# Kernel tuning notes

Hardware: AMD Instinct MI355X
Metric: run time of the kernel (lower is better)

Reference implementation:

```python
import jax, jax.numpy as jnp
import numpy as np

N = 100000   # nodes
E = 1250000  # edges
IN, HID, OUT = 64, 128, 32


def _gcn_norm(edge_index, num_nodes):
    # add self loops, unit edge weights, symmetric normalization (PyG gcn_norm)
    loops = jnp.arange(num_nodes, dtype=edge_index.dtype)
    src = jnp.concatenate([edge_index[0], loops])
    dst = jnp.concatenate([edge_index[1], loops])
    w = jnp.ones(src.shape[0], dtype=jnp.float32)
    deg = jax.ops.segment_sum(w, dst, num_segments=num_nodes)  # degree at targets
    dis = jnp.where(deg > 0, jax.lax.rsqrt(deg), 0.0)
    norm = dis[src] * dis[dst]  # per-edge coefficient
    return src, dst, norm


def _gcn_conv(h, W, b, src, dst, norm, num_nodes):
    hw = h @ W                                 # [N, out] linear transform first
    msg = hw[src] * norm[:, None]              # gather + scale  [E+N, out]
    agg = jax.ops.segment_sum(msg, dst, num_segments=num_nodes)
    return agg + b


def setup_inputs() -> dict:
    key = jax.random.key(0)
    ks = jax.random.split(key, 8)
    x = jax.random.normal(ks[0], (N, IN), dtype=jnp.float32)
    edge_index = jax.random.randint(ks[1], (2, E), 0, N, dtype=jnp.int32)
    def glorot(k, fan_in, fan_out):
        s = np.sqrt(6.0 / (fan_in + fan_out)).astype(np.float32)
        return jax.random.uniform(k, (fan_in, fan_out), jnp.float32, -s, s)
    return {
        "x": x,
        "edge_index": edge_index,
        "W1": glorot(ks[2], IN, HID),   "b1": jnp.zeros((HID,), jnp.float32),
        "W_mu": glorot(ks[3], HID, OUT), "b_mu": jnp.zeros((OUT,), jnp.float32),
        "W_lv": glorot(ks[4], HID, OUT), "b_lv": jnp.zeros((OUT,), jnp.float32),
    }


def reference(x, edge_index, W1, b1, W_mu, b_mu, W_lv, b_lv):
    src, dst, norm = _gcn_norm(edge_index, N)
    h = _gcn_conv(x, W1, b1, src, dst, norm, N)
    h = jax.nn.selu(h)
    # dropout: eval mode (training=False) -> identity
    mu = _gcn_conv(h, W_mu, b_mu, src, dst, norm, N)
    logvar = _gcn_conv(h, W_lv, b_lv, src, dst, norm, N)
    return (mu, logvar)
```

## Files before the change

### kernel.cpp

```cpp
#include <hip/hip_runtime.h>
#include <math.h>

#define NN 100000
#define NE 1250000
#define DIN 64
#define DHID 128
#define DO2 64
#define DOUT 32

#define NBIN 256
#define BINW ((NN + NBIN - 1) / NBIN)
#define PADW2 2752
#define P1_THREADS 1024
#define P1_EPT 8
#define P1_EPB (P1_THREADS * P1_EPT)

typedef unsigned int uint;
typedef unsigned short ushort;
typedef __attribute__((ext_vector_type(8))) short bf16x8;
typedef __attribute__((ext_vector_type(4))) float f32x4;

#define MFMA16(A, B, C) __builtin_amdgcn_mfma_f32_16x16x32_bf16(A, B, C, 0, 0, 0)

__device__ __forceinline__ ushort f2bf(float f) {
    uint u = __float_as_uint(f);
    uint r = (u + 0x7fffu + ((u >> 16) & 1u)) >> 16;
    return (ushort)r;
}
__device__ __forceinline__ uint pack2(float a, float b) {
    return (uint)f2bf(a) | ((uint)f2bf(b) << 16);
}
__device__ __forceinline__ float bflo(uint p) { return __uint_as_float(p << 16); }
__device__ __forceinline__ float bfhi(uint p) { return __uint_as_float(p & 0xffff0000u); }

__device__ __forceinline__ int nofk(int k) {
    return (k & 3) | (((k >> 3) & 3) << 2) | (((k >> 2) & 1) << 4) | ((k >> 5) << 5);
}

__global__ void zero_arr(int* a, int n) {
    int i = blockIdx.x * blockDim.x + threadIdx.x;
    if (i < n) a[i] = 0;
}

__global__ void cast_x(const float* __restrict__ x, const float* __restrict__ dis,
                       uint* __restrict__ xb, int npairs) {
    int i = blockIdx.x * blockDim.x + threadIdx.x;
    if (i < npairs) {
        int row = i >> 5;
        if (row < NN) {
            float dv = dis[row];
            float2 v = ((const float2*)x)[i];
            xb[i] = pack2(dv * v.x, dv * v.y);
        } else xb[i] = 0;
    }
}

__global__ __launch_bounds__(P1_THREADS) void bin_hist(const int* __restrict__ dst,
                                                       int* __restrict__ binhist, int n) {
    __shared__ int hist[NBIN];
    int tid = threadIdx.x;
    if (tid < NBIN) hist[tid] = 0;
    __syncthreads();
    int base = blockIdx.x * P1_EPB;
#pragma unroll
    for (int j = 0; j < P1_EPT; j++) {
        int i = base + j * P1_THREADS + tid;
        if (i < n) atomicAdd(&hist[dst[i] / BINW], 1);
    }
    __syncthreads();
    if (tid < NBIN) {
        int v = hist[tid];
        if (v) atomicAdd(&binhist[tid], v);
    }
}

__global__ __launch_bounds__(NBIN) void bin_scan(const int* __restrict__ binhist,
                                                 int* __restrict__ binoff,
                                                 int* __restrict__ bincur) {
    __shared__ int buf[NBIN];
    int tid = threadIdx.x;
    int v = binhist[tid];
    buf[tid] = v;
    __syncthreads();
    for (int off = 1; off < NBIN; off <<= 1) {
        int t = (tid >= off) ? buf[tid - off] : 0;
        __syncthreads();
        buf[tid] += t;
        __syncthreads();
    }
    int ex = buf[tid] - v;
    binoff[tid] = ex;
    bincur[tid] = ex;
    if (tid == NBIN - 1) binoff[NBIN] = buf[tid];
}

__global__ __launch_bounds__(P1_THREADS) void scatter_pass1(const int* __restrict__ src,
                                                            const int* __restrict__ dst,
                                                            int* __restrict__ bincur,
                                                            uint* __restrict__ ebin, int n) {
    __shared__ int hist[NBIN];
    __shared__ int gbase[NBIN];
    int tid = threadIdx.x;
    if (tid < NBIN) hist[tid] = 0;
    __syncthreads();
    int base = blockIdx.x * P1_EPB;
    uint e[P1_EPT];
    int  rk[P1_EPT];
    int  bn[P1_EPT];
#pragma unroll
    for (int j = 0; j < P1_EPT; j++) {
        int i = base + j * P1_THREADS + tid;
        if (i < n) {
            int d = dst[i];
            int b = d / BINW;
            e[j] = ((uint)src[i] << 9) | (uint)(d - b * BINW);
            bn[j] = b;
            rk[j] = atomicAdd(&hist[b], 1);
        } else bn[j] = -1;
    }
    __syncthreads();
    if (tid < NBIN) gbase[tid] = hist[tid] ? atomicAdd(&bincur[tid], hist[tid]) : 0;
    __syncthreads();
#pragma unroll
    for (int j = 0; j < P1_EPT; j++)
        if (bn[j] >= 0) ebin[gbase[bn[j]] + rk[j]] = e[j];
}

__global__ __launch_bounds__(256) void bin_finalize(const uint* __restrict__ ebin,
                                                    const int* __restrict__ binoff,
                                                    float* __restrict__ dis,
                                                    int* __restrict__ poffsets,
                                                    int* __restrict__ pends,
                                                    int* __restrict__ esrc) {
    __shared__ int hh[BINW];
    __shared__ int base_s[BINW];
    __shared__ int cur_s[BINW];
    int b = blockIdx.x;
    int tid = threadIdx.x;
    int v0 = b * BINW;
    int nv = min(BINW, NN - v0);
    int beg = binoff[b], end = binoff[b + 1];
    int pbase = ((beg + 7) & ~7) + PADW2 * b;
    for (int i = tid; i < nv; i += 256) { hh[i] = 0; cur_s[i] = 0; }
    __syncthreads();
    for (int i = beg + tid; i < end; i += 256)
        atomicAdd(&hh[ebin[i] & 511u], 1);
    __syncthreads();
    int i1 = tid + 256;
    int c0 = (tid < nv) ? hh[tid] : 0;  int p0 = (c0 + 7) & ~7;
    int c1 = (i1 < nv) ? hh[i1] : 0;    int p1 = (c1 + 7) & ~7;
    __syncthreads();
    if (tid < nv) hh[tid] = p0;
    if (i1 < nv) hh[i1] = p1;
    __syncthreads();
    for (int off = 1; off < BINW; off <<= 1) {
        int t0 = (tid < nv && tid >= off) ? hh[tid - off] : 0;
        int t1 = (i1 < nv && i1 >= off) ? hh[i1 - off] : 0;
        __syncthreads();
        if (tid < nv) hh[tid] += t0;
        if (i1 < nv) hh[i1] += t1;
        __syncthreads();
    }
    if (tid < nv) {
        int base = pbase + hh[tid] - p0;
        base_s[tid] = base;
        poffsets[v0 + tid] = base;
        pends[v0 + tid] = base + p0;
        dis[v0 + tid] = rsqrtf((float)c0 + 1.0f);
        for (int j = c0; j < p0; j++) esrc[base + j] = NN;
    }
    if (i1 < nv) {
        int base = pbase + hh[i1] - p1;
        base_s[i1] = base;
        poffsets[v0 + i1] = base;
        pends[v0 + i1] = base + p1;
        dis[v0 + i1] = rsqrtf((float)c1 + 1.0f);
        for (int j = c1; j < p1; j++) esrc[base + j] = NN;
    }
    __syncthreads();
    for (int i = beg + tid; i < end; i += 256) {
        uint e = ebin[i];
        int l = (int)(e & 511u);
        int pos = base_s[l] + atomicAdd(&cur_s[l], 1);
        esrc[pos] = (int)(e >> 9);
    }
}

__global__ void prep_weights(const float* __restrict__ W1, const float* __restrict__ Wmu,
                             const float* __restrict__ Wlv, ushort* __restrict__ Wall) {
    int i = blockIdx.x * blockDim.x + threadIdx.x;
    if (i >= 16384) return;
    if (i < 8192) {
        int lane = (i >> 3) & 63, e = i & 7;
        int fr = i >> 9;
        int t = fr >> 1, ks = fr & 1;
        int row = 16 * t + (lane & 15);
        int k = ks * 32 + (lane >> 4) * 8 + e;
        float w = W1[k * DHID + row];
        ushort hi = f2bf(w);
        Wall[i] = hi;
        Wall[8192 + i] = f2bf(w - bflo((uint)hi));
    } else {
        int ii = i - 8192;
        int lane = (ii >> 3) & 63, e = ii & 7;
        int fr = ii >> 9;
        int t2 = fr >> 2, ks = fr & 3;
        int nout = 16 * t2 + (lane & 15);
        int kpos = ks * 32 + (lane >> 4) * 8 + e;
        int h = nofk(kpos);
        float w = (nout < DOUT) ? Wmu[h * DOUT + nout] : Wlv[h * DOUT + (nout - DOUT)];
        ushort hi = f2bf(w);
        Wall[16384 + ii] = hi;
        Wall[24576 + ii] = f2bf(w - bflo((uint)hi));
    }
}

__global__ __launch_bounds__(256) void aggregateX(const uint* __restrict__ xsb,
                                                  const int* __restrict__ poffsets,
                                                  const int* __restrict__ pends,
                                                  const int* __restrict__ esrc,
                                                  const float* __restrict__ dis,
                                                  uint* __restrict__ axb) {
    int wave = threadIdx.x >> 6;
    int lane = threadIdx.x & 63;
    int oct  = lane >> 3;
    int j4   = (lane & 7) * 4;
    int v = blockIdx.x * 4 + wave;
    if (v >= NN) return;
    int beg = poffsets[v], end = pends[v];
    float a0 = 0.f, a1 = 0.f, a2 = 0.f, a3 = 0.f, a4 = 0.f, a5 = 0.f, a6 = 0.f, a7 = 0.f;
    for (int e0 = beg; e0 < end; e0 += 8) {
        int s = esrc[e0 + oct];
        uint4 p = *(const uint4*)(xsb + (size_t)s * 32 + j4);
        a0 += bflo(p.x); a1 += bfhi(p.x);
        a2 += bflo(p.y); a3 += bfhi(p.y);
        a4 += bflo(p.z); a5 += bfhi(p.z);
        a6 += bflo(p.w); a7 += bfhi(p.w);
    }
#pragma unroll
    for (int m = 8; m < 64; m <<= 1) {
        a0 += __shfl_xor(a0, m); a1 += __shfl_xor(a1, m);
        a2 += __shfl_xor(a2, m); a3 += __shfl_xor(a3, m);
        a4 += __shfl_xor(a4, m); a5 += __shfl_xor(a5, m);
        a6 += __shfl_xor(a6, m); a7 += __shfl_xor(a7, m);
    }
    uint4 pv = *(const uint4*)(xsb + (size_t)v * 32 + j4);
    a0 += bflo(pv.x); a1 += bfhi(pv.x);
    a2 += bflo(pv.y); a3 += bfhi(pv.y);
    a4 += bflo(pv.z); a5 += bfhi(pv.z);
    a6 += bflo(pv.w); a7 += bfhi(pv.w);
    if (lane < 8) {
        float dv = dis[v];
        uint4 o;
        o.x = pack2(dv * a0, dv * a1);
        o.y = pack2(dv * a2, dv * a3);
        o.z = pack2(dv * a4, dv * a5);
        o.w = pack2(dv * a6, dv * a7);
        *(uint4*)(axb + (size_t)v * 32 + j4) = o;
    }
}

__device__ __forceinline__ float selu_f(float v) {
    const float scale = 1.0507009873554805f;
    const float alpha = 1.6732632423543772f;
    return scale * (v > 0.f ? v : alpha * (expf(v) - 1.f));
}

__global__ __launch_bounds__(256) void gemm_fused(const uint* __restrict__ axb,
                                                  const ushort* __restrict__ Wall,
                                                  const float* __restrict__ b1,
                                                  const float* __restrict__ dis,
                                                  uint* __restrict__ hw2s) {
    __shared__ ushort Wlds[32768];
    int tid = threadIdx.x;
    int lane = tid & 63;
    int xr = lane & 15, q = lane >> 4;
    int rowbase = blockIdx.x * 128 + (tid >> 6) * 16;
    int v0 = rowbase + xr;
    int v1 = rowbase + 64 + xr;
    int v0c = min(v0, NN - 1);
    int v1c = min(v1, NN - 1);

    bf16x8 bf0[2], bf1[2];
#pragma unroll
    for (int ks = 0; ks < 2; ks++) {
        bf0[ks] = *(const bf16x8*)(axb + (size_t)v0c * 32 + ks * 16 + q * 4);
        bf1[ks] = *(const bf16x8*)(axb + (size_t)v1c * 32 + ks * 16 + q * 4);
    }

    {
        const uint4* wsrc = (const uint4*)Wall;
        uint4* wdst = (uint4*)Wlds;
#pragma unroll
        for (int c = 0; c < 16; c++) wdst[tid + c * 256] = wsrc[tid + c * 256];
    }
    __syncthreads();

    const char* ldsb = (const char*)Wlds;
    int lane16 = lane * 16;

    uint px0[8], py0[8], px1[8], py1[8];
#pragma unroll
    for (int t = 0; t < 8; t++) {
        bf16x8 ah0 = *(const bf16x8*)(ldsb + (t * 2 + 0) * 1024 + lane16);
        bf16x8 ah1 = *(const bf16x8*)(ldsb + (t * 2 + 1) * 1024 + lane16);
        bf16x8 al0 = *(const bf16x8*)(ldsb + 16384 + (t * 2 + 0) * 1024 + lane16);
        bf16x8 al1 = *(const bf16x8*)(ldsb + 16384 + (t * 2 + 1) * 1024 + lane16);
        f32x4 acc0 = {0.f, 0.f, 0.f, 0.f};
        f32x4 acc1 = {0.f, 0.f, 0.f, 0.f};
        acc0 = MFMA16(ah0, bf0[0], acc0); acc0 = MFMA16(al0, bf0[0], acc0);
        acc0 = MFMA16(ah1, bf0[1], acc0); acc0 = MFMA16(al1, bf0[1], acc0);
        acc1 = MFMA16(ah0, bf1[0], acc1); acc1 = MFMA16(al0, bf1[0], acc1);
        acc1 = MFMA16(ah1, bf1[1], acc1); acc1 = MFMA16(al1, bf1[1], acc1);
        float4 bb = *(const float4*)(b1 + 16 * t + 4 * q);
        px0[t] = pack2(selu_f(acc0[0] + bb.x), selu_f(acc0[1] + bb.y));
        py0[t] = pack2(selu_f(acc0[2] + bb.z), selu_f(acc0[3] + bb.w));
        px1[t] = pack2(selu_f(acc1[0] + bb.x), selu_f(acc1[1] + bb.y));
        py1[t] = pack2(selu_f(acc1[2] + bb.z), selu_f(acc1[3] + bb.w));
    }

    float dv0 = dis[v0c], dv1 = dis[v1c];
#pragma unroll
    for (int t2 = 0; t2 < 4; t2++) {
        f32x4 a0 = {0.f, 0.f, 0.f, 0.f};
        f32x4 a1 = {0.f, 0.f, 0.f, 0.f};
#pragma unroll
        for (int ks = 0; ks < 4; ks++) {
            bf16x8 ah = *(const bf16x8*)(ldsb + 32768 + (t2 * 4 + ks) * 1024 + lane16);
            bf16x8 al = *(const bf16x8*)(ldsb + 49152 + (t2 * 4 + ks) * 1024 + lane16);
            bf16x8 fr0, fr1;
            *(uint4*)&fr0 = make_uint4(px0[2 * ks], py0[2 * ks], px0[2 * ks + 1], py0[2 * ks + 1]);
            *(uint4*)&fr1 = make_uint4(px1[2 * ks], py1[2 * ks], px1[2 * ks + 1], py1[2 * ks + 1]);
            a0 = MFMA16(ah, fr0, a0); a0 = MFMA16(al, fr0, a0);
            a1 = MFMA16(ah, fr1, a1); a1 = MFMA16(al, fr1, a1);
        }
        if (v0 < NN) {
            uint2 pk;
            pk.x = pack2(dv0 * a0[0], dv0 * a0[1]);
            pk.y = pack2(dv0 * a0[2], dv0 * a0[3]);
            *(uint2*)(hw2s + (size_t)v0 * 32 + t2 * 8 + q * 2) = pk;
        }
        if (v1 < NN) {
            uint2 pk;
            pk.x = pack2(dv1 * a1[0], dv1 * a1[1]);
            pk.y = pack2(dv1 * a1[2], dv1 * a1[3]);
            *(uint2*)(hw2s + (size_t)v1 * 32 + t2 * 8 + q * 2) = pk;
        }
    }
}

__global__ __launch_bounds__(256) void aggregate2(const uint* __restrict__ hw2s,
                                                  const int* __restrict__ poffsets,
                                                  const int* __restrict__ pends,
                                                  const int* __restrict__ esrc,
                                                  const float* __restrict__ dis,
                                                  const float* __restrict__ bmu,
                                                  const float* __restrict__ blv,
                                                  float* __restrict__ out) {
    int wave = threadIdx.x >> 6;
    int lane = threadIdx.x & 63;
    int oct  = lane >> 3;
    int j4   = (lane & 7) * 4;
    int v = blockIdx.x * 4 + wave;
    if (v >= NN) return;
    int beg = poffsets[v], end = pends[v];
    float a0 = 0.f, a1 = 0.f, a2 = 0.f, a3 = 0.f, a4 = 0.f, a5 = 0.f, a6 = 0.f, a7 = 0.f;
    for (int e0 = beg; e0 < end; e0 += 8) {
        int s = esrc[e0 + oct];
        uint4 p = *(const uint4*)(hw2s + (size_t)s * 32 + j4);
        a0 += bflo(p.x); a1 += bfhi(p.x);
        a2 += bflo(p.y); a3 += bfhi(p.y);
        a4 += bflo(p.z); a5 += bfhi(p.z);
        a6 += bflo(p.w); a7 += bfhi(p.w);
    }
#pragma unroll
    for (int m = 8; m < 64; m <<= 1) {
        a0 += __shfl_xor(a0, m); a1 += __shfl_xor(a1, m);
        a2 += __shfl_xor(a2, m); a3 += __shfl_xor(a3, m);
        a4 += __shfl_xor(a4, m); a5 += __shfl_xor(a5, m);
        a6 += __shfl_xor(a6, m); a7 += __shfl_xor(a7, m);
    }
    uint4 pv = *(const uint4*)(hw2s + (size_t)v * 32 + j4);
    a0 += bflo(pv.x); a1 += bfhi(pv.x);
    a2 += bflo(pv.y); a3 += bfhi(pv.y);
    a4 += bflo(pv.z); a5 += bfhi(pv.z);
    a6 += bflo(pv.w); a7 += bfhi(pv.w);
    if (lane < 8) {
        float dv = dis[v];
        int j = lane;
        const float* bp = (j < 4) ? (bmu + 8 * j) : (blv + 8 * j - 32);
        float* op = (j < 4) ? (out + (size_t)v * DOUT + 8 * j)
                            : (out + (size_t)NN * DOUT + (size_t)v * DOUT + 8 * j - 32);
        float4 b0 = *(const float4*)bp;
        float4 b1 = *(const float4*)(bp + 4);
        *(float4*)op       = make_float4(dv * a0 + b0.x, dv * a1 + b0.y,
                                         dv * a2 + b0.z, dv * a3 + b0.w);
        *(float4*)(op + 4) = make_float4(dv * a4 + b1.x, dv * a5 + b1.y,
                                         dv * a6 + b1.z, dv * a7 + b1.w);
    }
}

extern "C" void kernel_launch(void* const* d_in, const int* in_sizes, int n_in,
                              void* d_out, int out_size, void* d_ws, size_t ws_size,
                              hipStream_t stream) {
    const float* x   = (const float*)d_in[0];
    const int*   ei  = (const int*)d_in[1];
    const int*   e_src = ei;
    const int*   e_dst = ei + NE;
    const float* W1  = (const float*)d_in[2];
    const float* b1  = (const float*)d_in[3];
    const float* Wmu = (const float*)d_in[4];
    const float* bmu = (const float*)d_in[5];
    const float* Wlv = (const float*)d_in[6];
    const float* blv = (const float*)d_in[7];
    float* out = (float*)d_out;

    char* ws = (char*)d_ws;
    size_t off = 0;
    auto alloc = [&](size_t bytes) -> void* {
        void* p = ws + off;
        off += (bytes + 255) & ~(size_t)255;
        return p;
    };
    int*    poffsets  = (int*)alloc((size_t)(NN + 1) * 4);
    int*    pends     = (int*)alloc((size_t)NN * 4);
    int*    esrc      = (int*)alloc((size_t)(NE + (size_t)PADW2 * NBIN + 64) * 4);
    int*    binhist   = (int*)alloc((size_t)NBIN * 4);
    int*    binoff    = (int*)alloc((size_t)(NBIN + 1) * 4);
    int*    bincur    = (int*)alloc((size_t)NBIN * 4);
    float*  dis       = (float*)alloc((size_t)NN * 4);
    ushort* Wall      = (ushort*)alloc((size_t)32768 * 2);
    uint*   xb        = (uint*)alloc((size_t)(NN + 1) * 32 * 4);
    uint*   axb       = (uint*)alloc((size_t)NN * 32 * 4);
    uint*   hw2s      = xb;
    uint*   ebin      = axb;

    int p1blocks = (NE + P1_EPB - 1) / P1_EPB;
    zero_arr<<<1, NBIN, 0, stream>>>(binhist, NBIN);
    bin_hist<<<p1blocks, P1_THREADS, 0, stream>>>(e_dst, binhist, NE);
    bin_scan<<<1, NBIN, 0, stream>>>(binhist, binoff, bincur);
    scatter_pass1<<<p1blocks, P1_THREADS, 0, stream>>>(e_src, e_dst, bincur, ebin, NE);
    bin_finalize<<<NBIN, 256, 0, stream>>>(ebin, binoff, dis, poffsets, pends, esrc);
    prep_weights<<<64, 256, 0, stream>>>(W1, Wmu, Wlv, Wall);
    cast_x<<<(((NN + 1) * 32) + 255) / 256, 256, 0, stream>>>(x, dis, xb, (NN + 1) * 32);

    aggregateX<<<(NN + 3) / 4, 256, 0, stream>>>(xb, poffsets, pends, esrc, dis, axb);
    gemm_fused<<<(NN + 127) / 128, 256, 0, stream>>>(axb, Wall, b1, dis, hw2s);
    aggregate2<<<(NN + 3) / 4, 256, 0, stream>>>(hw2s, poffsets, pends, esrc, dis, bmu, blv, out);
}
```

Measured before the change: 242.7 us.

## Preload edge indices per wave, dual accumulators in aggregation, fuse prep kernels

Both aggregation kernels now load up to 64 neighbour indices with one coalesced read per wave and pass them to lanes with shuffles. They also unroll by two with separate accumulators so more gathers are in flight at once, and they issue the self-row and dis loads early. The begin and end offsets are merged into one int2 array, prep_weights and cast_x become a single launch, and the zeroing kernel is replaced by hipMemsetAsync. The aim is to cut launch overhead and per-edge index-load latency on a gather-bound path, at the cost of more registers per thread.

```diff
diff --git a/kernel.cpp b/kernel.cpp
--- a/kernel.cpp
+++ b/kernel.cpp
@@ -37,23 +37,11 @@
     return (k & 3) | (((k >> 3) & 3) << 2) | (((k >> 2) & 1) << 4) | ((k >> 5) << 5);
 }
 
-__global__ void zero_arr(int* a, int n) {
-    int i = blockIdx.x * blockDim.x + threadIdx.x;
-    if (i < n) a[i] = 0;
-}
-
-__global__ void cast_x(const float* __restrict__ x, const float* __restrict__ dis,
-                       uint* __restrict__ xb, int npairs) {
-    int i = blockIdx.x * blockDim.x + threadIdx.x;
-    if (i < npairs) {
-        int row = i >> 5;
-        if (row < NN) {
-            float dv = dis[row];
-            float2 v = ((const float2*)x)[i];
-            xb[i] = pack2(dv * v.x, dv * v.y);
-        } else xb[i] = 0;
-    }
-}
+#define ACC8(A, P) do { \
+    A##0 += bflo((P).x); A##1 += bfhi((P).x); \
+    A##2 += bflo((P).y); A##3 += bfhi((P).y); \
+    A##4 += bflo((P).z); A##5 += bfhi((P).z); \
+    A##6 += bflo((P).w); A##7 += bfhi((P).w); } while (0)
 
 __global__ __launch_bounds__(P1_THREADS) void bin_hist(const int* __restrict__ dst,
                                                        int* __restrict__ binhist, int n) {
@@ -129,8 +117,7 @@
 __global__ __launch_bounds__(256) void bin_finalize(const uint* __restrict__ ebin,
                                                     const int* __restrict__ binoff,
                                                     float* __restrict__ dis,
-                                                    int* __restrict__ poffsets,
-                                                    int* __restrict__ pends,
+                                                    int2* __restrict__ prange,
                                                     int* __restrict__ esrc) {
     __shared__ int hh[BINW];
     __shared__ int base_s[BINW];
@@ -164,16 +151,14 @@
     if (tid < nv) {
         int base = pbase + hh[tid] - p0;
         base_s[tid] = base;
-        poffsets[v0 + tid] = base;
-        pends[v0 + tid] = base + p0;
+        prange[v0 + tid] = make_int2(base, base + p0);
         dis[v0 + tid] = rsqrtf((float)c0 + 1.0f);
         for (int j = c0; j < p0; j++) esrc[base + j] = NN;
     }
     if (i1 < nv) {
         int base = pbase + hh[i1] - p1;
         base_s[i1] = base;
-        poffsets[v0 + i1] = base;
-        pends[v0 + i1] = base + p1;
+        prange[v0 + i1] = make_int2(base, base + p1);
         dis[v0 + i1] = rsqrtf((float)c1 + 1.0f);
         for (int j = c1; j < p1; j++) esrc[base + j] = NN;
     }
@@ -186,38 +171,51 @@
     }
 }
 
-__global__ void prep_weights(const float* __restrict__ W1, const float* __restrict__ Wmu,
-                             const float* __restrict__ Wlv, ushort* __restrict__ Wall) {
-    int i = blockIdx.x * blockDim.x + threadIdx.x;
-    if (i >= 16384) return;
-    if (i < 8192) {
-        int lane = (i >> 3) & 63, e = i & 7;
-        int fr = i >> 9;
-        int t = fr >> 1, ks = fr & 1;
-        int row = 16 * t + (lane & 15);
-        int k = ks * 32 + (lane >> 4) * 8 + e;
-        float w = W1[k * DHID + row];
-        ushort hi = f2bf(w);
-        Wall[i] = hi;
-        Wall[8192 + i] = f2bf(w - bflo((uint)hi));
+__global__ void prep_and_cast(const float* __restrict__ x, const float* __restrict__ dis,
+                              uint* __restrict__ xb,
+                              const float* __restrict__ W1, const float* __restrict__ Wmu,
+                              const float* __restrict__ Wlv, ushort* __restrict__ Wall) {
+    int bi = blockIdx.x;
+    if (bi < 64) {
+        int i = bi * 256 + threadIdx.x;
+        if (i < 8192) {
+            int lane = (i >> 3) & 63, e = i & 7;
+            int fr = i >> 9;
+            int t = fr >> 1, ks = fr & 1;
+            int row = 16 * t + (lane & 15);
+            int k = ks * 32 + (lane >> 4) * 8 + e;
+            float w = W1[k * DHID + row];
+            ushort hi = f2bf(w);
+            Wall[i] = hi;
+            Wall[8192 + i] = f2bf(w - bflo((uint)hi));
+        } else {
+            int ii = i - 8192;
+            int lane = (ii >> 3) & 63, e = ii & 7;
+            int fr = ii >> 9;
+            int t2 = fr >> 2, ks = fr & 3;
+            int nout = 16 * t2 + (lane & 15);
+            int kpos = ks * 32 + (lane >> 4) * 8 + e;
+            int h = nofk(kpos);
+            float w = (nout < DOUT) ? Wmu[h * DOUT + nout] : Wlv[h * DOUT + (nout - DOUT)];
+            ushort hi = f2bf(w);
+            Wall[16384 + ii] = hi;
+            Wall[24576 + ii] = f2bf(w - bflo((uint)hi));
+        }
     } else {
-        int ii = i - 8192;
-        int lane = (ii >> 3) & 63, e = ii & 7;
-        int fr = ii >> 9;
-        int t2 = fr >> 2, ks = fr & 3;
-        int nout = 16 * t2 + (lane & 15);
-        int kpos = ks * 32 + (lane >> 4) * 8 + e;
-        int h = nofk(kpos);
-        float w = (nout < DOUT) ? Wmu[h * DOUT + nout] : Wlv[h * DOUT + (nout - DOUT)];
-        ushort hi = f2bf(w);
-        Wall[16384 + ii] = hi;
-        Wall[24576 + ii] = f2bf(w - bflo((uint)hi));
+        int i = (bi - 64) * 256 + threadIdx.x;
+        if (i < (NN + 1) * 32) {
+            int row = i >> 5;
+            if (row < NN) {
+                float dv = dis[row];
+                float2 v = ((const float2*)x)[i];
+                xb[i] = pack2(dv * v.x, dv * v.y);
+            } else xb[i] = 0;
+        }
     }
 }
 
 __global__ __launch_bounds__(256) void aggregateX(const uint* __restrict__ xsb,
-                                                  const int* __restrict__ poffsets,
-                                                  const int* __restrict__ pends,
+                                                  const int2* __restrict__ prange,
                                                   const int* __restrict__ esrc,
                                                   const float* __restrict__ dis,
                                                   uint* __restrict__ axb) {
@@ -227,16 +225,35 @@
     int j4   = (lane & 7) * 4;
     int v = blockIdx.x * 4 + wave;
     if (v >= NN) return;
-    int beg = poffsets[v], end = pends[v];
+    int2 rng = prange[v];
+    int beg = rng.x, nb = rng.y - rng.x;
+    uint4 pv = *(const uint4*)(xsb + (size_t)v * 32 + j4);
+    float dv = dis[v];
+    int sreg = (lane < nb) ? esrc[beg + lane] : NN;
     float a0 = 0.f, a1 = 0.f, a2 = 0.f, a3 = 0.f, a4 = 0.f, a5 = 0.f, a6 = 0.f, a7 = 0.f;
-    for (int e0 = beg; e0 < end; e0 += 8) {
-        int s = esrc[e0 + oct];
+    float b0 = 0.f, b1 = 0.f, b2 = 0.f, b3 = 0.f, b4 = 0.f, b5 = 0.f, b6 = 0.f, b7 = 0.f;
+    int ncap = min(nb, 64);
+    int g = 0;
+    for (; g + 16 <= ncap; g += 16) {
+        int sA = __shfl(sreg, g + oct);
+        int sB = __shfl(sreg, g + 8 + oct);
+        uint4 pA = *(const uint4*)(xsb + (size_t)sA * 32 + j4);
+        uint4 pB = *(const uint4*)(xsb + (size_t)sB * 32 + j4);
+        ACC8(a, pA);
+        ACC8(b, pB);
+    }
+    if (g < ncap) {
+        int sA = __shfl(sreg, g + oct);
+        uint4 pA = *(const uint4*)(xsb + (size_t)sA * 32 + j4);
+        ACC8(a, pA);
+        g += 8;
+    }
+    for (; g < nb; g += 8) {
+        int s = esrc[beg + g + oct];
         uint4 p = *(const uint4*)(xsb + (size_t)s * 32 + j4);
-        a0 += bflo(p.x); a1 += bfhi(p.x);
-        a2 += bflo(p.y); a3 += bfhi(p.y);
-        a4 += bflo(p.z); a5 += bfhi(p.z);
-        a6 += bflo(p.w); a7 += bfhi(p.w);
-    }
+        ACC8(b, p);
+    }
+    a0 += b0; a1 += b1; a2 += b2; a3 += b3; a4 += b4; a5 += b5; a6 += b6; a7 += b7;
 #pragma unroll
     for (int m = 8; m < 64; m <<= 1) {
         a0 += __shfl_xor(a0, m); a1 += __shfl_xor(a1, m);
@@ -244,13 +261,8 @@
         a4 += __shfl_xor(a4, m); a5 += __shfl_xor(a5, m);
         a6 += __shfl_xor(a6, m); a7 += __shfl_xor(a7, m);
     }
-    uint4 pv = *(const uint4*)(xsb + (size_t)v * 32 + j4);
-    a0 += bflo(pv.x); a1 += bfhi(pv.x);
-    a2 += bflo(pv.y); a3 += bfhi(pv.y);
-    a4 += bflo(pv.z); a5 += bfhi(pv.z);
-    a6 += bflo(pv.w); a7 += bfhi(pv.w);
+    ACC8(a, pv);
     if (lane < 8) {
-        float dv = dis[v];
         uint4 o;
         o.x = pack2(dv * a0, dv * a1);
         o.y = pack2(dv * a2, dv * a3);
@@ -350,8 +362,7 @@
 }
 
 __global__ __launch_bounds__(256) void aggregate2(const uint* __restrict__ hw2s,
-                                                  const int* __restrict__ poffsets,
-                                                  const int* __restrict__ pends,
+                                                  const int2* __restrict__ prange,
                                                   const int* __restrict__ esrc,
                                                   const float* __restrict__ dis,
                                                   const float* __restrict__ bmu,
@@ -363,16 +374,35 @@
     int j4   = (lane & 7) * 4;
     int v = blockIdx.x * 4 + wave;
     if (v >= NN) return;
-    int beg = poffsets[v], end = pends[v];
+    int2 rng = prange[v];
+    int beg = rng.x, nb = rng.y - rng.x;
+    uint4 pv = *(const uint4*)(hw2s + (size_t)v * 32 + j4);
+    float dv = dis[v];
+    int sreg = (lane < nb) ? esrc[beg + lane] : NN;
     float a0 = 0.f, a1 = 0.f, a2 = 0.f, a3 = 0.f, a4 = 0.f, a5 = 0.f, a6 = 0.f, a7 = 0.f;
-    for (int e0 = beg; e0 < end; e0 += 8) {
-        int s = esrc[e0 + oct];
+    float b0 = 0.f, b1 = 0.f, b2 = 0.f, b3 = 0.f, b4 = 0.f, b5 = 0.f, b6 = 0.f, b7 = 0.f;
+    int ncap = min(nb, 64);
+    int g = 0;
+    for (; g + 16 <= ncap; g += 16) {
+        int sA = __shfl(sreg, g + oct);
+        int sB = __shfl(sreg, g + 8 + oct);
+        uint4 pA = *(const uint4*)(hw2s + (size_t)sA * 32 + j4);
+        uint4 pB = *(const uint4*)(hw2s + (size_t)sB * 32 + j4);
+        ACC8(a, pA);
+        ACC8(b, pB);
+    }
+    if (g < ncap) {
+        int sA = __shfl(sreg, g + oct);
+        uint4 pA = *(const uint4*)(hw2s + (size_t)sA * 32 + j4);
+        ACC8(a, pA);
+        g += 8;
+    }
+    for (; g < nb; g += 8) {
+        int s = esrc[beg + g + oct];
         uint4 p = *(const uint4*)(hw2s + (size_t)s * 32 + j4);
-        a0 += bflo(p.x); a1 += bfhi(p.x);
-        a2 += bflo(p.y); a3 += bfhi(p.y);
-        a4 += bflo(p.z); a5 += bfhi(p.z);
-        a6 += bflo(p.w); a7 += bfhi(p.w);
-    }
+        ACC8(b, p);
+    }
+    a0 += b0; a1 += b1; a2 += b2; a3 += b3; a4 += b4; a5 += b5; a6 += b6; a7 += b7;
 #pragma unroll
     for (int m = 8; m < 64; m <<= 1) {
         a0 += __shfl_xor(a0, m); a1 += __shfl_xor(a1, m);
@@ -380,23 +410,18 @@
         a4 += __shfl_xor(a4, m); a5 += __shfl_xor(a5, m);
         a6 += __shfl_xor(a6, m); a7 += __shfl_xor(a7, m);
     }
-    uint4 pv = *(const uint4*)(hw2s + (size_t)v * 32 + j4);
-    a0 += bflo(pv.x); a1 += bfhi(pv.x);
-    a2 += bflo(pv.y); a3 += bfhi(pv.y);
-    a4 += bflo(pv.z); a5 += bfhi(pv.z);
-    a6 += bflo(pv.w); a7 += bfhi(pv.w);
+    ACC8(a, pv);
     if (lane < 8) {
-        float dv = dis[v];
         int j = lane;
         const float* bp = (j < 4) ? (bmu + 8 * j) : (blv + 8 * j - 32);
         float* op = (j < 4) ? (out + (size_t)v * DOUT + 8 * j)
                             : (out + (size_t)NN * DOUT + (size_t)v * DOUT + 8 * j - 32);
-        float4 b0 = *(const float4*)bp;
-        float4 b1 = *(const float4*)(bp + 4);
-        *(float4*)op       = make_float4(dv * a0 + b0.x, dv * a1 + b0.y,
-                                         dv * a2 + b0.z, dv * a3 + b0.w);
-        *(float4*)(op + 4) = make_float4(dv * a4 + b1.x, dv * a5 + b1.y,
-                                         dv * a6 + b1.z, dv * a7 + b1.w);
+        float4 c0 = *(const float4*)bp;
+        float4 c1 = *(const float4*)(bp + 4);
+        *(float4*)op       = make_float4(dv * a0 + c0.x, dv * a1 + c0.y,
+                                         dv * a2 + c0.z, dv * a3 + c0.w);
+        *(float4*)(op + 4) = make_float4(dv * a4 + c1.x, dv * a5 + c1.y,
+                                         dv * a6 + c1.z, dv * a7 + c1.w);
     }
 }
 
@@ -422,8 +447,7 @@
         off += (bytes + 255) & ~(size_t)255;
         return p;
     };
-    int*    poffsets  = (int*)alloc((size_t)(NN + 1) * 4);
-    int*    pends     = (int*)alloc((size_t)NN * 4);
+    int2*   prange    = (int2*)alloc((size_t)NN * 8);
     int*    esrc      = (int*)alloc((size_t)(NE + (size_t)PADW2 * NBIN + 64) * 4);
     int*    binhist   = (int*)alloc((size_t)NBIN * 4);
     int*    binoff    = (int*)alloc((size_t)(NBIN + 1) * 4);
@@ -436,15 +460,15 @@
     uint*   ebin      = axb;
 
     int p1blocks = (NE + P1_EPB - 1) / P1_EPB;
-    zero_arr<<<1, NBIN, 0, stream>>>(binhist, NBIN);
+    hipMemsetAsync(binhist, 0, NBIN * 4, stream);
     bin_hist<<<p1blocks, P1_THREADS, 0, stream>>>(e_dst, binhist, NE);
     bin_scan<<<1, NBIN, 0, stream>>>(binhist, binoff, bincur);
     scatter_pass1<<<p1blocks, P1_THREADS, 0, stream>>>(e_src, e_dst, bincur, ebin, NE);
-    bin_finalize<<<NBIN, 256, 0, stream>>>(ebin, binoff, dis, poffsets, pends, esrc);
-    prep_weights<<<64, 256, 0, stream>>>(W1, Wmu, Wlv, Wall);
-    cast_x<<<(((NN + 1) * 32) + 255) / 256, 256, 0, stream>>>(x, dis, xb, (NN + 1) * 32);
-
-    aggregateX<<<(NN + 3) / 4, 256, 0, stream>>>(xb, poffsets, pends, esrc, dis, axb);
+    bin_finalize<<<NBIN, 256, 0, stream>>>(ebin, binoff, dis, prange, esrc);
+    prep_and_cast<<<64 + (((NN + 1) * 32) + 255) / 256, 256, 0, stream>>>(
+        x, dis, xb, W1, Wmu, Wlv, Wall);
+
+    aggregateX<<<(NN + 3) / 4, 256, 0, stream>>>(xb, prange, esrc, dis, axb);
     gemm_fused<<<(NN + 127) / 128, 256, 0, stream>>>(axb, Wall, b1, dis, hw2s);
-    aggregate2<<<(NN + 3) / 4, 256, 0, stream>>>(hw2s, poffsets, pends, esrc, dis, bmu, blv, out);
-}
+    aggregate2<<<(NN + 3) / 4, 256, 0, stream>>>(hw2s, prange, esrc, dis, bmu, blv, out);
+}
```

Result: faster. 229.0 us (-5.6%).
